# Optimization experiments

Hardware: AMD Instinct MI355X
Metric: run time of the kernel (lower is better)

Reference implementation:

```python
import jax, jax.numpy as jnp
import numpy as np

# dims: T time steps, B batch, CIN/COUT conv channels, HxW spatial, K kernel
T, B, CIN, COUT, H, Wd, K = 10, 32, 3, 64, 64, 64, 3
DECAY = 0.2      # LIF leak factor
INH = 1.625      # lateral inhibition strength (mode='threshold')


def setup_inputs() -> dict:
    key = jax.random.key(0)
    k1, k2 = jax.random.split(key)
    x = (jax.random.uniform(k1, (T, B, CIN, H, Wd)) < 0.2).astype(jnp.float32)
    W = jax.random.normal(k2, (COUT, CIN, K, K), dtype=jnp.float32)
    # normweight(): zero-mean, unit-std (biased) per output filter
    W = W - W.mean(axis=(1, 2, 3), keepdims=True)
    W = W / W.reshape(COUT, -1).std(axis=1).reshape(COUT, 1, 1, 1)
    return {"x": x, "W": W}


def _conv(x, W):
    # Conv2d stride=1, padding=1, no bias, NCHW/OIHW
    return jax.lax.conv_general_dilated(
        x, W, window_strides=(1, 1), padding=((1, 1), (1, 1)),
        dimension_numbers=("NCHW", "OIHW", "NCHW"))


def reference(x, W):
    def step(mem, x_t):
        i = _conv(x_t, W)                                        # (B,COUT,H,W)
        # ATB: adaptive per-channel threshold = max over batch+spatial
        thr = jnp.max(i, axis=(0, 2, 3), keepdims=True) + 1e-4   # (1,COUT,1,1)
        # ASF: clamp then thresholded sigmoid filter
        cur = jnp.maximum(i, 0.0)
        i_asf = thr * jax.nn.sigmoid((cur - 0.4 * thr) * (8.0 / thr))
        # LIF update with threshold = thr (set by ATB)
        mem = mem * DECAY + i_asf
        s = (mem > thr).astype(mem.dtype)                        # spikes 0/1
        # WTA k=1: keep only the strongest spiking channel per location
        score = mem * s
        winner = jnp.argmax(score, axis=1)                       # (B,H,W)
        oh = jnp.moveaxis(jax.nn.one_hot(winner, COUT, dtype=mem.dtype), -1, 1)
        s = s * oh
        # membrane reset of fired neurons
        mem = mem * (1.0 - s)
        # lateral inhibition: suppress non-winners at spiking locations
        any_sp = jnp.max(s, axis=1, keepdims=True)
        mem = mem - INH * thr * any_sp * (1.0 - s)
        return mem, s

    mem0 = jnp.zeros((B, COUT, H, Wd), jnp.float32)
    _, spikes = jax.lax.scan(step, mem0, x)
    return spikes  # (T,B,COUT,H,W)
```

## Files before the change

kernel.cpp:

```cpp
#include <hip/hip_runtime.h>
#include <math.h>

#define TT 10
#define BB 32
#define CIN 3
#define COUT 64
#define HH 64
#define WW 64
#define HW (HH*WW)
#define DECAY 0.2f
#define INH 1.625f
#define RS 68

__device__ __forceinline__ unsigned int enc_f(float f) {
    unsigned int u = __float_as_uint(f);
    return (u & 0x80000000u) ? ~u : (u | 0x80000000u);
}
__device__ __forceinline__ float dec_f(unsigned int u) {
    u = (u & 0x80000000u) ? (u & 0x7FFFFFFFu) : ~u;
    return __uint_as_float(u);
}

template <int NROWS, int RPC>
__device__ __forceinline__ void stage_x(float* sxf, const float* xb,
                                        int ghbase, int tid) {
    const int NSLOT = NROWS * RS;
    const int NITER = (NSLOT + 255) / 256;
    float vals[NITER];
    #pragma unroll
    for (int it = 0; it < NITER; it++) {
        int l = tid + it * 256;
        float v = 0.f;
        if (l < NSLOT) {
            int row = l / RS, cl = l % RS;
            int ci = row / RPC, rr = row % RPC;
            int gh = ghbase + rr - 1;
            if (cl >= 1 && cl <= 64 && gh >= 0 && gh < HH)
                v = xb[ci * HW + gh * WW + (cl - 1)];
        }
        vals[it] = v;
    }
    #pragma unroll
    for (int it = 0; it < NITER; it++) {
        int l = tid + it * 256;
        if (l < NSLOT) sxf[l] = vals[it];
    }
}

__device__ __forceinline__ void conv16(const float* __restrict__ sxbase,
                                       const int* rows, const float* w,
                                       int p0, float acc[16]) {
    #pragma unroll
    for (int j = 0; j < 16; j++) acc[j] = 0.f;
    #pragma unroll
    for (int q = 0; q < 9; q++) {
        const float* rp = sxbase + rows[q] * RS + p0;
        float xr[18];
        float4 a0 = *(const float4*)(rp + 0);
        float4 a1 = *(const float4*)(rp + 4);
        float4 a2 = *(const float4*)(rp + 8);
        float4 a3 = *(const float4*)(rp + 12);
        float2 a4 = *(const float2*)(rp + 16);
        xr[0]=a0.x; xr[1]=a0.y; xr[2]=a0.z; xr[3]=a0.w;
        xr[4]=a1.x; xr[5]=a1.y; xr[6]=a1.z; xr[7]=a1.w;
        xr[8]=a2.x; xr[9]=a2.y; xr[10]=a2.z; xr[11]=a2.w;
        xr[12]=a3.x; xr[13]=a3.y; xr[14]=a3.z; xr[15]=a3.w;
        xr[16]=a4.x; xr[17]=a4.y;
        const float w0 = w[q * 3 + 0];
        const float w1 = w[q * 3 + 1];
        const float w2 = w[q * 3 + 2];
        #pragma unroll
        for (int j = 0; j < 16; j++) {
            acc[j] = fmaf(w0, xr[j],     acc[j]);
            acc[j] = fmaf(w1, xr[j + 1], acc[j]);
            acc[j] = fmaf(w2, xr[j + 2], acc[j]);
        }
    }
}

__global__ __launch_bounds__(256) void thr_kernel(
    const float* __restrict__ x,
    const float* __restrict__ Wt,
    unsigned int* __restrict__ thr_raw)
{
    __shared__ float sx[CIN * 6][RS];
    __shared__ float wmax[4][COUT];

    const int tid  = threadIdx.x;
    const int lane = tid & 63;
    const int wave = tid >> 6;
    const int h0   = blockIdx.x * 4;
    const int b    = blockIdx.y;
    const int t    = blockIdx.z;

    float w[27];
    #pragma unroll
    for (int k = 0; k < 27; k++) w[k] = Wt[lane * 27 + k];

    const float* xb = x + ((size_t)t * BB + b) * (CIN * HW);
    stage_x<CIN * 6, 6>(&sx[0][0], xb, h0, tid);
    __syncthreads();

    int rows[9];
    #pragma unroll
    for (int ci = 0; ci < CIN; ci++)
        #pragma unroll
        for (int kh = 0; kh < 3; kh++)
            rows[ci * 3 + kh] = ci * 6 + wave + kh;

    float mx = -INFINITY;
    #pragma unroll 1
    for (int cc = 0; cc < 4; cc++) {
        float acc[16];
        conv16(&sx[0][0], rows, w, cc * 16, acc);
        float m01 = fmaxf(fmaxf(acc[0], acc[1]), fmaxf(acc[2], acc[3]));
        float m23 = fmaxf(fmaxf(acc[4], acc[5]), fmaxf(acc[6], acc[7]));
        float m45 = fmaxf(fmaxf(acc[8], acc[9]), fmaxf(acc[10], acc[11]));
        float m67 = fmaxf(fmaxf(acc[12], acc[13]), fmaxf(acc[14], acc[15]));
        mx = fmaxf(mx, fmaxf(fmaxf(m01, m23), fmaxf(m45, m67)));
    }

    wmax[wave][lane] = mx;
    __syncthreads();
    if (wave == 0) {
        float m = fmaxf(fmaxf(wmax[0][lane], wmax[1][lane]),
                        fmaxf(wmax[2][lane], wmax[3][lane]));
        atomicMax(&thr_raw[t * COUT + lane], enc_f(m));
    }
}

__global__ __launch_bounds__(256) void lif_kernel(
    const float* __restrict__ x,
    const float* __restrict__ Wt,
    const unsigned int* __restrict__ thr_raw,
    float* __restrict__ out)
{
    __shared__ float sx[CIN * 3][RS];

    const int tid  = threadIdx.x;
    const int lane = tid & 63;
    const int wave = tid >> 6;
    const int p0   = __builtin_amdgcn_readfirstlane(wave * 16);
    const int b    = blockIdx.x >> 6;
    const int h    = blockIdx.x & 63;

    float w[27];
    #pragma unroll
    for (int k = 0; k < 27; k++) w[k] = Wt[lane * 27 + k];

    int rows[9];
    #pragma unroll
    for (int q = 0; q < 9; q++) rows[q] = q;

    float mem[16];
    #pragma unroll
    for (int j = 0; j < 16; j++) mem[j] = 0.f;

    #pragma unroll 1
    for (int t = 0; t < TT; t++) {
        __syncthreads();

        const float* xb = x + ((size_t)t * BB + b) * (CIN * HW);
        stage_x<CIN * 3, 3>(&sx[0][0], xb, h, tid);

        float thr   = dec_f(thr_raw[t * COUT + lane]) + 1e-4f;
        float sinv  = 8.0f / thr;
        float s04   = 0.4f * thr;
        float sinh_ = INH * thr;
        __syncthreads();

        float acc[16];
        conv16(&sx[0][0], rows, w, p0, acc);

        int fmask = 0, amask = 0;
        #pragma unroll
        for (int j = 0; j < 16; j++) {
            float cur = fmaxf(acc[j], 0.f);
            float z   = (cur - s04) * sinv;
            float sig = 1.0f / (1.0f + expf(-z));
            float m   = mem[j] * DECAY + thr * sig;
            int   sp  = m > thr;
            float score = sp ? m : 0.f;

            unsigned long long blt = __ballot(sp);
            int fr = 0, sp_any = 0;
            if (blt) {
                float bs = score;
                int   bc = lane;
                #pragma unroll
                for (int off = 32; off > 0; off >>= 1) {
                    float so = __shfl_xor(bs, off, 64);
                    int   co = __shfl_xor(bc, off, 64);
                    if (so > bs || (so == bs && co < bc)) { bs = so; bc = co; }
                }
                sp_any = __shfl(sp, bc, 64);
                fr     = (lane == bc) && sp;
            }
            mem[j] = fr ? 0.f : (m - (sp_any ? sinh_ : 0.f));
            if (fr) fmask |= (1 << j);
            if (sp_any) amask |= (1 << j);
        }

        float* ob = out + (((size_t)t * BB + b) * COUT + lane) * HW
                        + h * WW + p0;
        #pragma unroll
        for (int g = 0; g < 4; g++) {
            float4 v;
            v.x = (fmask >> (g * 4 + 0)) & 1 ? 1.f : 0.f;
            v.y = (fmask >> (g * 4 + 1)) & 1 ? 1.f : 0.f;
            v.z = (fmask >> (g * 4 + 2)) & 1 ? 1.f : 0.f;
            v.w = (fmask >> (g * 4 + 3)) & 1 ? 1.f : 0.f;
            *(float4*)(ob + g * 4) = v;
        }
    }
}

extern "C" void kernel_launch(void* const* d_in, const int* in_sizes, int n_in,
                              void* d_out, int out_size, void* d_ws, size_t ws_size,
                              hipStream_t stream) {
    const float* x = (const float*)d_in[0];
    const float* W = (const float*)d_in[1];
    float* out     = (float*)d_out;

    unsigned int* thr = (unsigned int*)d_ws;
    hipMemsetAsync(thr, 0, TT * COUT * sizeof(unsigned int), stream);

    thr_kernel<<<dim3(HH / 4, BB, TT), 256, 0, stream>>>(x, W, thr);
    lif_kernel<<<dim3(BB * HH), 256, 0, stream>>>(x, W, thr, out);
}
```

Before: 556.9 us.

## Materialize conv output in workspace instead of recomputing it in LIF kernel

The convolution was computed twice: once to find the per-channel max threshold and again inside the LIF kernel. Now the conv kernel stores all conv outputs to a large workspace buffer in [b][h][w][cout] layout, and the LIF kernel only streams those values. This removes the repeated convolution and the input staging in the LIF pass. The cost is writing and then reading a float buffer as large as the output. If the workspace is too small, it falls back to per-timestep conv/LIF launch pairs that carry the membrane state through global memory.

```diff
diff --git a/kernel.cpp b/kernel.cpp
--- a/kernel.cpp
+++ b/kernel.cpp
@@ -11,6 +11,7 @@
 #define DECAY 0.2f
 #define INH 1.625f
 #define RS 68
+#define ISLAB ((size_t)HW * COUT)
 
 __device__ __forceinline__ unsigned int enc_f(float f) {
     unsigned int u = __float_as_uint(f);
@@ -78,10 +79,12 @@
     }
 }
 
-__global__ __launch_bounds__(256) void thr_kernel(
+__global__ __launch_bounds__(256) void conv_kernel(
     const float* __restrict__ x,
     const float* __restrict__ Wt,
-    unsigned int* __restrict__ thr_raw)
+    float* __restrict__ ibuf,
+    unsigned int* __restrict__ thr_raw,
+    int t0)
 {
     __shared__ float sx[CIN * 6][RS];
     __shared__ float wmax[4][COUT];
@@ -91,7 +94,7 @@
     const int wave = tid >> 6;
     const int h0   = blockIdx.x * 4;
     const int b    = blockIdx.y;
-    const int t    = blockIdx.z;
+    const int t    = t0 + blockIdx.z;
 
     float w[27];
     #pragma unroll
@@ -107,17 +110,20 @@
         #pragma unroll
         for (int kh = 0; kh < 3; kh++)
             rows[ci * 3 + kh] = ci * 6 + wave + kh;
+
+    float* ist = ibuf + ((size_t)blockIdx.z * BB + b) * ISLAB
+                      + (size_t)(h0 + wave) * WW * COUT;
 
     float mx = -INFINITY;
     #pragma unroll 1
     for (int cc = 0; cc < 4; cc++) {
         float acc[16];
         conv16(&sx[0][0], rows, w, cc * 16, acc);
-        float m01 = fmaxf(fmaxf(acc[0], acc[1]), fmaxf(acc[2], acc[3]));
-        float m23 = fmaxf(fmaxf(acc[4], acc[5]), fmaxf(acc[6], acc[7]));
-        float m45 = fmaxf(fmaxf(acc[8], acc[9]), fmaxf(acc[10], acc[11]));
-        float m67 = fmaxf(fmaxf(acc[12], acc[13]), fmaxf(acc[14], acc[15]));
-        mx = fmaxf(mx, fmaxf(fmaxf(m01, m23), fmaxf(m45, m67)));
+        #pragma unroll
+        for (int j = 0; j < 16; j++) {
+            ist[(size_t)(cc * 16 + j) * COUT + lane] = acc[j];
+            mx = fmaxf(mx, acc[j]);
+        }
     }
 
     wmax[wave][lane] = mx;
@@ -129,14 +135,13 @@
     }
 }
 
-__global__ __launch_bounds__(256) void lif_kernel(
-    const float* __restrict__ x,
-    const float* __restrict__ Wt,
+__global__ __launch_bounds__(256) void lif_stream(
+    const float* __restrict__ ibuf,
     const unsigned int* __restrict__ thr_raw,
-    float* __restrict__ out)
+    float* __restrict__ out,
+    float* __restrict__ memws,
+    int t0, int nt)
 {
-    __shared__ float sx[CIN * 3][RS];
-
     const int tid  = threadIdx.x;
     const int lane = tid & 63;
     const int wave = tid >> 6;
@@ -144,38 +149,34 @@
     const int b    = blockIdx.x >> 6;
     const int h    = blockIdx.x & 63;
 
-    float w[27];
-    #pragma unroll
-    for (int k = 0; k < 27; k++) w[k] = Wt[lane * 27 + k];
-
-    int rows[9];
-    #pragma unroll
-    for (int q = 0; q < 9; q++) rows[q] = q;
+    float* mrow = memws + ((size_t)b * HH + h) * WW * COUT;
 
     float mem[16];
-    #pragma unroll
-    for (int j = 0; j < 16; j++) mem[j] = 0.f;
+    if (t0 == 0) {
+        #pragma unroll
+        for (int j = 0; j < 16; j++) mem[j] = 0.f;
+    } else {
+        #pragma unroll
+        for (int j = 0; j < 16; j++)
+            mem[j] = mrow[(size_t)(p0 + j) * COUT + lane];
+    }
 
     #pragma unroll 1
-    for (int t = 0; t < TT; t++) {
-        __syncthreads();
-
-        const float* xb = x + ((size_t)t * BB + b) * (CIN * HW);
-        stage_x<CIN * 3, 3>(&sx[0][0], xb, h, tid);
+    for (int tt = 0; tt < nt; tt++) {
+        const int t = t0 + tt;
+        const float* ild = ibuf + ((size_t)tt * BB + b) * ISLAB
+                                + (size_t)h * WW * COUT;
 
         float thr   = dec_f(thr_raw[t * COUT + lane]) + 1e-4f;
         float sinv  = 8.0f / thr;
         float s04   = 0.4f * thr;
         float sinh_ = INH * thr;
-        __syncthreads();
-
-        float acc[16];
-        conv16(&sx[0][0], rows, w, p0, acc);
-
-        int fmask = 0, amask = 0;
+
+        int fmask = 0;
         #pragma unroll
         for (int j = 0; j < 16; j++) {
-            float cur = fmaxf(acc[j], 0.f);
+            float iv  = ild[(size_t)(p0 + j) * COUT + lane];
+            float cur = fmaxf(iv, 0.f);
             float z   = (cur - s04) * sinv;
             float sig = 1.0f / (1.0f + expf(-z));
             float m   = mem[j] * DECAY + thr * sig;
@@ -198,7 +199,6 @@
             }
             mem[j] = fr ? 0.f : (m - (sp_any ? sinh_ : 0.f));
             if (fr) fmask |= (1 << j);
-            if (sp_any) amask |= (1 << j);
         }
 
         float* ob = out + (((size_t)t * BB + b) * COUT + lane) * HW
@@ -213,6 +213,12 @@
             *(float4*)(ob + g * 4) = v;
         }
     }
+
+    if (t0 + nt < TT) {
+        #pragma unroll
+        for (int j = 0; j < 16; j++)
+            mrow[(size_t)(p0 + j) * COUT + lane] = mem[j];
+    }
 }
 
 extern "C" void kernel_launch(void* const* d_in, const int* in_sizes, int n_in,
@@ -222,9 +228,25 @@
     const float* W = (const float*)d_in[1];
     float* out     = (float*)d_out;
 
-    unsigned int* thr = (unsigned int*)d_ws;
+    char* ws = (char*)d_ws;
+    unsigned int* thr = (unsigned int*)ws;
+    const size_t IOFF  = 65536;
+    const size_t SLABB = ISLAB * sizeof(float);
+
     hipMemsetAsync(thr, 0, TT * COUT * sizeof(unsigned int), stream);
 
-    thr_kernel<<<dim3(HH / 4, BB, TT), 256, 0, stream>>>(x, W, thr);
-    lif_kernel<<<dim3(BB * HH), 256, 0, stream>>>(x, W, thr, out);
-}
+    if (ws_size >= IOFF + TT * SLABB) {
+        float* ibuf = (float*)(ws + IOFF);
+        conv_kernel<<<dim3(HH / 4, BB, TT), 256, 0, stream>>>(x, W, ibuf, thr, 0);
+        lif_stream<<<dim3(BB * HH), 256, 0, stream>>>(ibuf, thr, out,
+                                                      (float*)(ws + IOFF), 0, TT);
+    } else {
+        float* ibuf  = (float*)(ws + IOFF);
+        float* memws = (float*)(ws + IOFF + SLABB);
+        for (int t = 0; t < TT; t++) {
+            conv_kernel<<<dim3(HH / 4, BB, 1), 256, 0, stream>>>(x, W, ibuf, thr, t);
+            lif_stream<<<dim3(BB * HH), 256, 0, stream>>>(ibuf, thr, out,
+                                                          memws, t, 1);
+        }
+    }
+}
```

New measurement: 667.4 us. 1.2x slower.

## Fuse threshold and LIF kernels into one cooperative kernel with grid sync

Applied to the files above, without the earlier changes.

Replaces the two-kernel scheme, which computed the convolution twice, with a single cooperative kernel. Each block computes the conv for two rows, stores the results in shared memory, and contributes per-channel maxima through atomics. A grid-wide sync follows, then the LIF/WTA step runs from the cached conv values. This removes the redundant conv pass and a kernel launch. In exchange it adds ten grid barriers, higher register and LDS use, and a check-before-atomicMax to reduce contention. The old kernels remain as a fallback if the cooperative launch fails.

```diff
diff --git a/kernel.cpp b/kernel.cpp
--- a/kernel.cpp
+++ b/kernel.cpp
@@ -1,5 +1,8 @@
 #include <hip/hip_runtime.h>
+#include <hip/hip_cooperative_groups.h>
 #include <math.h>
+
+namespace cg = cooperative_groups;
 
 #define TT 10
 #define BB 32
@@ -78,9 +81,129 @@
     }
 }
 
-__global__ __launch_bounds__(256) void thr_kernel(
+__global__ __launch_bounds__(256, 4) void snn_coop(
     const float* __restrict__ x,
     const float* __restrict__ Wt,
+    float* __restrict__ out,
+    unsigned int* __restrict__ thr_raw)
+{
+    __shared__ float sx[12][RS];
+    __shared__ float sI[128][64];
+    __shared__ float wmax[4][COUT];
+
+    cg::grid_group grid = cg::this_grid();
+
+    const int tid  = threadIdx.x;
+    const int lane = tid & 63;
+    const int wave = tid >> 6;
+    const int row  = wave >> 1;
+    const int p0   = __builtin_amdgcn_readfirstlane((wave & 1) * 32);
+    const int b    = blockIdx.x >> 5;
+    const int h0   = (blockIdx.x & 31) * 2;
+    const int h    = h0 + row;
+
+    float w[27];
+    #pragma unroll
+    for (int k = 0; k < 27; k++) w[k] = Wt[lane * 27 + k];
+
+    int rows[9];
+    #pragma unroll
+    for (int ci = 0; ci < CIN; ci++)
+        #pragma unroll
+        for (int kh = 0; kh < 3; kh++)
+            rows[ci * 3 + kh] = ci * 4 + row + kh;
+
+    float mem[32];
+    #pragma unroll
+    for (int j = 0; j < 32; j++) mem[j] = 0.f;
+
+    #pragma unroll 1
+    for (int t = 0; t < TT; t++) {
+        __syncthreads();
+
+        const float* xb = x + ((size_t)t * BB + b) * (CIN * HW);
+        stage_x<12, 4>(&sx[0][0], xb, h0, tid);
+        __syncthreads();
+
+        float mx = -INFINITY;
+        #pragma unroll 1
+        for (int cc = 0; cc < 2; cc++) {
+            float acc[16];
+            conv16(&sx[0][0], rows, w, p0 + cc * 16, acc);
+            #pragma unroll
+            for (int j = 0; j < 16; j++) {
+                sI[row * 64 + p0 + cc * 16 + j][lane] = acc[j];
+                mx = fmaxf(mx, acc[j]);
+            }
+        }
+        wmax[wave][lane] = mx;
+        __syncthreads();
+
+        if (wave == 0) {
+            float m = fmaxf(fmaxf(wmax[0][lane], wmax[1][lane]),
+                            fmaxf(wmax[2][lane], wmax[3][lane]));
+            unsigned int e = enc_f(m);
+            unsigned int cur = __hip_atomic_load(&thr_raw[t * COUT + lane],
+                                                 __ATOMIC_RELAXED,
+                                                 __HIP_MEMORY_SCOPE_AGENT);
+            if (e > cur) atomicMax(&thr_raw[t * COUT + lane], e);
+        }
+
+        grid.sync();
+
+        unsigned int u = __hip_atomic_load(&thr_raw[t * COUT + lane],
+                                           __ATOMIC_RELAXED,
+                                           __HIP_MEMORY_SCOPE_AGENT);
+        float thr   = dec_f(u) + 1e-4f;
+        float sinv  = 8.0f / thr;
+        float s04   = 0.4f * thr;
+        float sinh_ = INH * thr;
+
+        unsigned int fmask = 0;
+        #pragma unroll
+        for (int j = 0; j < 32; j++) {
+            float iv  = sI[row * 64 + p0 + j][lane];
+            float cur = fmaxf(iv, 0.f);
+            float z   = (cur - s04) * sinv;
+            float sig = 1.0f / (1.0f + expf(-z));
+            float m   = mem[j] * DECAY + thr * sig;
+            int   sp  = m > thr;
+            float score = sp ? m : 0.f;
+
+            unsigned long long blt = __ballot(sp);
+            int fr = 0, sp_any = 0;
+            if (blt) {
+                float bs = score;
+                int   bc = lane;
+                #pragma unroll
+                for (int off = 32; off > 0; off >>= 1) {
+                    float so = __shfl_xor(bs, off, 64);
+                    int   co = __shfl_xor(bc, off, 64);
+                    if (so > bs || (so == bs && co < bc)) { bs = so; bc = co; }
+                }
+                sp_any = __shfl(sp, bc, 64);
+                fr     = (lane == bc) && sp;
+            }
+            mem[j] = fr ? 0.f : (m - (sp_any ? sinh_ : 0.f));
+            if (fr) fmask |= (1u << j);
+        }
+
+        float* ob = out + (((size_t)t * BB + b) * COUT + lane) * HW
+                        + h * WW + p0;
+        #pragma unroll
+        for (int g = 0; g < 8; g++) {
+            float4 v;
+            v.x = (fmask >> (g * 4 + 0)) & 1 ? 1.f : 0.f;
+            v.y = (fmask >> (g * 4 + 1)) & 1 ? 1.f : 0.f;
+            v.z = (fmask >> (g * 4 + 2)) & 1 ? 1.f : 0.f;
+            v.w = (fmask >> (g * 4 + 3)) & 1 ? 1.f : 0.f;
+            *(float4*)(ob + g * 4) = v;
+        }
+    }
+}
+
+__global__ __launch_bounds__(256) void thr_kernel(
+    const float* __restrict__ x, const float* __restrict__ Wt,
     unsigned int* __restrict__ thr_raw)
 {
     __shared__ float sx[CIN * 6][RS];
@@ -113,11 +236,8 @@
     for (int cc = 0; cc < 4; cc++) {
         float acc[16];
         conv16(&sx[0][0], rows, w, cc * 16, acc);
-        float m01 = fmaxf(fmaxf(acc[0], acc[1]), fmaxf(acc[2], acc[3]));
-        float m23 = fmaxf(fmaxf(acc[4], acc[5]), fmaxf(acc[6], acc[7]));
-        float m45 = fmaxf(fmaxf(acc[8], acc[9]), fmaxf(acc[10], acc[11]));
-        float m67 = fmaxf(fmaxf(acc[12], acc[13]), fmaxf(acc[14], acc[15]));
-        mx = fmaxf(mx, fmaxf(fmaxf(m01, m23), fmaxf(m45, m67)));
+        #pragma unroll
+        for (int j = 0; j < 16; j++) mx = fmaxf(mx, acc[j]);
     }
 
     wmax[wave][lane] = mx;
@@ -130,10 +250,8 @@
 }
 
 __global__ __launch_bounds__(256) void lif_kernel(
-    const float* __restrict__ x,
-    const float* __restrict__ Wt,
-    const unsigned int* __restrict__ thr_raw,
-    float* __restrict__ out)
+    const float* __restrict__ x, const float* __restrict__ Wt,
+    const unsigned int* __restrict__ thr_raw, float* __restrict__ out)
 {
     __shared__ float sx[CIN * 3][RS];
 
@@ -159,10 +277,8 @@
     #pragma unroll 1
     for (int t = 0; t < TT; t++) {
         __syncthreads();
-
         const float* xb = x + ((size_t)t * BB + b) * (CIN * HW);
         stage_x<CIN * 3, 3>(&sx[0][0], xb, h, tid);
-
         float thr   = dec_f(thr_raw[t * COUT + lane]) + 1e-4f;
         float sinv  = 8.0f / thr;
         float s04   = 0.4f * thr;
@@ -172,7 +288,7 @@
         float acc[16];
         conv16(&sx[0][0], rows, w, p0, acc);
 
-        int fmask = 0, amask = 0;
+        int fmask = 0;
         #pragma unroll
         for (int j = 0; j < 16; j++) {
             float cur = fmaxf(acc[j], 0.f);
@@ -181,7 +297,6 @@
             float m   = mem[j] * DECAY + thr * sig;
             int   sp  = m > thr;
             float score = sp ? m : 0.f;
-
             unsigned long long blt = __ballot(sp);
             int fr = 0, sp_any = 0;
             if (blt) {
@@ -198,7 +313,6 @@
             }
             mem[j] = fr ? 0.f : (m - (sp_any ? sinh_ : 0.f));
             if (fr) fmask |= (1 << j);
-            if (sp_any) amask |= (1 << j);
         }
 
         float* ob = out + (((size_t)t * BB + b) * COUT + lane) * HW
@@ -225,6 +339,13 @@
     unsigned int* thr = (unsigned int*)d_ws;
     hipMemsetAsync(thr, 0, TT * COUT * sizeof(unsigned int), stream);
 
-    thr_kernel<<<dim3(HH / 4, BB, TT), 256, 0, stream>>>(x, W, thr);
-    lif_kernel<<<dim3(BB * HH), 256, 0, stream>>>(x, W, thr, out);
-}
+    void* args[] = { (void*)&x, (void*)&W, (void*)&out, (void*)&thr };
+    hipError_t err = hipLaunchCooperativeKernel((void*)snn_coop,
+                                                dim3(1024), dim3(256),
+                                                args, 0, stream);
+    if (err != hipSuccess) {
+        (void)hipGetLastError();
+        thr_kernel<<<dim3(HH / 4, BB, TT), 256, 0, stream>>>(x, W, thr);
+        lif_kernel<<<dim3(BB * HH), 256, 0, stream>>>(x, W, thr, out);
+    }
+}
```

Measured after the change: 1.784 ms. +220.3%, slower.
